# Kernel optimization log

Hardware: AMD Instinct MI355X
Metric: run time of the kernel (lower is better)

The kernel has to match this reference:

```python
import jax, jax.numpy as jnp
import numpy as np

B, S = 32, 256          # batch, sequence
D = 128                 # d_model
I = 256                 # mamba intermediate = 2*D
N = 16                  # ssm state size
R = 8                   # dt rank = ceil(D/16)
K = 4                   # conv kernel
L = 4                   # num mamba layers
Z = 128                 # vib z_dim
FUT = 20                # future steps


def setup_inputs() -> dict:
    key = jax.random.key(0)
    ks = iter(jax.random.split(key, 40))

    def nrm(shape, scale=0.02):
        return jax.random.normal(next(ks), shape, dtype=jnp.float32) * scale

    return {
        "x_cam": jax.random.normal(next(ks), (B, S, 8, 1024), dtype=jnp.float32),
        "x_ego": jax.random.normal(next(ks), (B, S, 64), dtype=jnp.float32),
        "vib_eps": jax.random.normal(next(ks), (B, Z), dtype=jnp.float32),
        "vis_w1": nrm((8 * 1024, 512)), "vis_b1": jnp.zeros((512,), jnp.float32),
        "vis_w2": nrm((512, D)), "vis_b2": jnp.zeros((D,), jnp.float32),
        "ego_w": nrm((64, D)), "ego_b": jnp.zeros((D,), jnp.float32),
        "fus_w": nrm((2 * D, D)), "fus_b": jnp.zeros((D,), jnp.float32),
        "norm_w": jnp.ones((L, D), jnp.float32),
        "in_proj_w": nrm((L, D, 2 * I)),
        "conv_w": nrm((L, I, K), 0.1), "conv_b": jnp.zeros((L, I), jnp.float32),
        "x_proj_w": nrm((L, I, R + 2 * N)),
        "dt_proj_w": nrm((L, R, I), 0.1), "dt_proj_b": jnp.full((L, I), -2.0, jnp.float32),
        "A_log": jnp.tile(jnp.log(jnp.arange(1, N + 1, dtype=jnp.float32))[None, None, :], (L, I, 1)),
        "D_par": jnp.ones((L, I), jnp.float32),
        "out_proj_w": nrm((L, I, D)),
        "normf_w": jnp.ones((D,), jnp.float32),
        "mu_w": nrm((D, Z)), "mu_b": jnp.zeros((Z,), jnp.float32),
        "lv_w": nrm((D, Z)), "lv_b": jnp.zeros((Z,), jnp.float32),
        "h1_w": nrm((Z, 256)), "h1_b": jnp.zeros((256,), jnp.float32),
        "h2_w": nrm((256, FUT * 2)), "h2_b": jnp.zeros((FUT * 2,), jnp.float32),
    }


def _rms(x, w, eps=1e-5):
    return x * jax.lax.rsqrt(jnp.mean(x * x, axis=-1, keepdims=True) + eps) * w


def _mixer(x, inw, cw, cb, xpw, dtw, dtb, alog, dpar, outw):
    # x: [B,S,D]
    Bb, Ss, _ = x.shape
    h, gate = jnp.split(x @ inw, 2, axis=-1)            # [B,S,I] each
    # depthwise causal conv (kernel K)
    hp = jnp.pad(h, ((0, 0), (K - 1, 0), (0, 0)))
    h = sum(hp[:, k:k + Ss, :] * cw[:, k] for k in range(K)) + cb
    h = jax.nn.silu(h)
    ssm = h @ xpw                                        # [B,S,R+2N]
    dt = jax.nn.softplus(ssm[..., :R] @ dtw + dtb)       # [B,S,I]
    Bm = ssm[..., R:R + N]                               # [B,S,N]
    Cm = ssm[..., R + N:]                                # [B,S,N]
    A = -jnp.exp(alog)                                   # [I,N]
    dA = jnp.exp(dt[..., None] * A)                      # [B,S,I,N]
    dBu = dt[..., None] * Bm[:, :, None, :] * h[..., None]  # [B,S,I,N]

    def step(carry, t):
        dA_t, dBu_t, C_t = t
        carry = carry * dA_t + dBu_t                     # [B,I,N]
        return carry, jnp.einsum('bin,bn->bi', carry, C_t)

    h0 = jnp.zeros((Bb, I, N), dtype=x.dtype)
    _, ys = jax.lax.scan(step, h0, (dA.swapaxes(0, 1), dBu.swapaxes(0, 1), Cm.swapaxes(0, 1)))
    y = ys.swapaxes(0, 1) + h * dpar                     # [B,S,I]
    y = y * jax.nn.silu(gate)
    return y @ outw                                      # [B,S,D]


def _mamba(x, norm_w, in_proj_w, conv_w, conv_b, x_proj_w, dt_proj_w, dt_proj_b, A_log, D_par, out_proj_w, normf_w):
    for l in range(L):
        x = x + _mixer(_rms(x, norm_w[l]), in_proj_w[l], conv_w[l], conv_b[l],
                       x_proj_w[l], dt_proj_w[l], dt_proj_b[l], A_log[l], D_par[l], out_proj_w[l])
    return _rms(x, normf_w)


def _forward(x_cam, x_ego, vib_eps, vis_w1, vis_b1, vis_w2, vis_b2, ego_w, ego_b, fus_w, fus_b,
             norm_w, in_proj_w, conv_w, conv_b, x_proj_w, dt_proj_w, dt_proj_b, A_log, D_par,
             out_proj_w, normf_w, mu_w, mu_b, lv_w, lv_b, h1_w, h1_b, h2_w, h2_b):
    Bb, Ss = x_cam.shape[:2]
    v = x_cam.reshape(Bb, Ss, -1)                                          # [B,S,8192]
    v = jax.nn.gelu(v @ vis_w1 + vis_b1, approximate=False) @ vis_w2 + vis_b2
    e = x_ego @ ego_w + ego_b
    fused = jax.nn.gelu(jnp.concatenate([v, e], axis=-1) @ fus_w + fus_b, approximate=False)
    h = _mamba(fused, norm_w, in_proj_w, conv_w, conv_b, x_proj_w,
               dt_proj_w, dt_proj_b, A_log, D_par, out_proj_w, normf_w)
    last = h[:, -1, :]                                                     # [B,D]
    mu = last @ mu_w + mu_b
    logvar = last @ lv_w + lv_b
    z = mu + vib_eps * jnp.exp(0.5 * logvar)
    kl = -0.5 * jnp.mean(1.0 + logvar - mu * mu - jnp.exp(logvar))
    out = jax.nn.relu(z @ h1_w + h1_b) @ h2_w + h2_b
    return out.reshape(Bb, FUT, 2), kl


def reference(x_cam, x_ego, vib_eps, vis_w1, vis_b1, vis_w2, vis_b2, ego_w, ego_b, fus_w, fus_b,
              norm_w, in_proj_w, conv_w, conv_b, x_proj_w, dt_proj_w, dt_proj_b, A_log, D_par,
              out_proj_w, normf_w, mu_w, mu_b, lv_w, lv_b, h1_w, h1_b, h2_w, h2_b):
    return _forward(x_cam, x_ego, vib_eps, vis_w1, vis_b1, vis_w2, vis_b2, ego_w, ego_b, fus_w, fus_b,
                    norm_w, in_proj_w, conv_w, conv_b, x_proj_w, dt_proj_w, dt_proj_b, A_log, D_par,
                    out_proj_w, normf_w, mu_w, mu_b, lv_w, lv_b, h1_w, h1_b, h2_w, h2_b)
```

## Files before the change

kernel.cpp:

```cpp
#include <hip/hip_runtime.h>
#include <hip/hip_bf16.h>
#include <math.h>

#define BQ 32
#define SQ 256
#define MTOK 8192
#define DD 128
#define II 256
#define NNs 16
#define RRs 8
#define KKs 4
#define LLs 4
#define ZZs 128
#define FUTs 20

typedef __attribute__((ext_vector_type(8))) short bf8v;
typedef __attribute__((ext_vector_type(4))) float f4v;

__device__ __forceinline__ float geluf(float x){ return 0.5f*x*(1.0f+erff(x*0.70710678118654752f)); }
__device__ __forceinline__ float siluf(float x){ return x/(1.0f+__expf(-x)); }
__device__ __forceinline__ float softplusf(float x){ return fmaxf(x,0.0f)+log1pf(__expf(-fabsf(x))); }
__device__ __forceinline__ unsigned short f2bf(float x){
    __hip_bfloat16 h = __float2bfloat16(x);
    return *reinterpret_cast<unsigned short*>(&h);
}

__device__ __forceinline__ void gload_lds16(const void* g, void* l){
    __builtin_amdgcn_global_load_lds(
        (const __attribute__((address_space(1))) void*)g,
        (__attribute__((address_space(3))) void*)l, 16, 0, 0);
}

#define PIPE_WAIT_BAR(N) do {                                   \
    __builtin_amdgcn_sched_barrier(0);                          \
    asm volatile("s_waitcnt vmcnt(" #N ")" ::: "memory");       \
    __builtin_amdgcn_s_barrier();                               \
    __builtin_amdgcn_sched_barrier(0);                          \
} while(0)

#define PIPE_END_BAR() do {                                     \
    __builtin_amdgcn_sched_barrier(0);                          \
    asm volatile("s_waitcnt lgkmcnt(0)" ::: "memory");          \
    __builtin_amdgcn_s_barrier();                               \
    __builtin_amdgcn_sched_barrier(0);                          \
} while(0)

template<int ACT,int ADD,int OUTBF>
__launch_bounds__(256,1)
__global__ void gemm_lds128_kernel(const unsigned short* __restrict__ A,
                                   const unsigned short* __restrict__ Bt,
                                   const float* __restrict__ bias,
                                   void* __restrict__ Cv,
                                   int M, int N, int Kd, int ldc)
{
    __shared__ __align__(16) unsigned short As[3][128*64];
    __shared__ __align__(16) unsigned short Bs[3][128*64];
    const int tid = threadIdx.x;
    const int w = tid >> 6, lane = tid & 63;
    const int ml = lane & 15, quad = lane >> 4;
    const int wm = w >> 1, wn = w & 1;
    const int rowBase = blockIdx.x * 128, colBase = blockIdx.y * 128;

    const int srow = w*8 + (lane>>3);
    const int scol = (((lane&7) ^ (lane>>3)))*8;

    f4v acc[4][4];
    #pragma unroll
    for (int i=0;i<4;i++)
      #pragma unroll
      for (int j=0;j<4;j++) acc[i][j] = (f4v){0.f,0.f,0.f,0.f};

    auto stage = [&](int buf, int kt){
        #pragma unroll
        for (int e=0;e<4;e++){
            const unsigned short* src = A + (size_t)(rowBase + srow + e*32)*Kd + kt + scol;
            gload_lds16(src, (unsigned short*)As[buf] + (w + e*4)*512);
        }
        #pragma unroll
        for (int e=0;e<4;e++){
            const unsigned short* src = Bt + (size_t)(colBase + srow + e*32)*Kd + kt + scol;
            gload_lds16(src, (unsigned short*)Bs[buf] + (w + e*4)*512);
        }
    };

    const int swz = (ml&7)*8;

    auto compute = [&](int buf){
        #pragma unroll
        for (int ks=0; ks<2; ks++){
            const int co = (ks*32 + quad*8) ^ swz;
            bf8v a[4], b[4];
            #pragma unroll
            for (int mf=0; mf<4; mf++)
                a[mf] = *reinterpret_cast<const bf8v*>(&As[buf][(wm*64 + mf*16 + ml)*64 + co]);
            #pragma unroll
            for (int nf=0; nf<4; nf++)
                b[nf] = *reinterpret_cast<const bf8v*>(&Bs[buf][(wn*64 + nf*16 + ml)*64 + co]);
            #pragma unroll
            for (int mf=0; mf<4; mf++)
                #pragma unroll
                for (int nf=0; nf<4; nf++)
                    acc[mf][nf] = __builtin_amdgcn_mfma_f32_16x16x32_bf16(a[mf], b[nf], acc[mf][nf], 0,0,0);
        }
    };

    const int nIter = Kd >> 6;
    stage(0, 0);
    stage(1, 64);

    int i = 0;
    for (; i + 2 < nIter; ++i){
        stage((i+2)%3, (i+2)<<6);
        PIPE_WAIT_BAR(16);
        compute(i%3);
        PIPE_END_BAR();
    }
    PIPE_WAIT_BAR(8);
    compute(i%3);
    PIPE_END_BAR();
    ++i;
    PIPE_WAIT_BAR(0);
    compute(i%3);

    #pragma unroll
    for (int mf=0; mf<4; mf++){
        #pragma unroll
        for (int nf=0; nf<4; nf++){
            int col = colBase + wn*64 + nf*16 + ml;
            float bb = bias ? bias[col] : 0.0f;
            #pragma unroll
            for (int r=0;r<4;r++){
                int row = rowBase + wm*64 + mf*16 + quad*4 + r;
                float v = acc[mf][nf][r] + bb;
                if (ACT==1) v = geluf(v);
                if constexpr (OUTBF==1){
                    ((unsigned short*)Cv)[(size_t)row*ldc + col] = f2bf(v);
                } else {
                    float* cp = (float*)Cv + (size_t)row*ldc + col;
                    if (ADD) v += *cp;
                    *cp = v;
                }
            }
        }
    }
}

template<int ACT,int ADD,int OUTBF>
__launch_bounds__(256,2)
__global__ void gemm_lds_kernel(const unsigned short* __restrict__ A,
                                const unsigned short* __restrict__ Bt,
                                const float* __restrict__ bias,
                                void* __restrict__ Cv,
                                int M, int N, int Kd, int ldc)
{
    __shared__ __align__(16) unsigned short As[3][128*64];
    __shared__ __align__(16) unsigned short Bs[3][64*64];
    const int tid = threadIdx.x;
    const int w = tid >> 6, lane = tid & 63;
    const int ml = lane & 15, quad = lane >> 4;
    const int rowBase = blockIdx.x * 128, colBase = blockIdx.y * 64;

    const int srow = w*8 + (lane>>3);
    const int scol = (((lane&7) ^ (lane>>3)))*8;

    f4v acc[2][4];
    #pragma unroll
    for (int i=0;i<2;i++)
      #pragma unroll
      for (int j=0;j<4;j++) acc[i][j] = (f4v){0.f,0.f,0.f,0.f};

    auto stage = [&](int buf, int kt){
        #pragma unroll
        for (int e=0;e<4;e++){
            const unsigned short* src = A + (size_t)(rowBase + srow + e*32)*Kd + kt + scol;
            gload_lds16(src, (unsigned short*)As[buf] + (w + e*4)*512);
        }
        #pragma unroll
        for (int e=0;e<2;e++){
            const unsigned short* src = Bt + (size_t)(colBase + srow + e*32)*Kd + kt + scol;
            gload_lds16(src, (unsigned short*)Bs[buf] + (w + e*4)*512);
        }
    };

    const int swz = (ml&7)*8;

    auto compute = [&](int buf){
        #pragma unroll
        for (int ks=0; ks<2; ks++){
            const int co = (ks*32 + quad*8) ^ swz;
            bf8v a0 = *reinterpret_cast<const bf8v*>(&As[buf][(w*32 +      ml)*64 + co]);
            bf8v a1 = *reinterpret_cast<const bf8v*>(&As[buf][(w*32 + 16 + ml)*64 + co]);
            #pragma unroll
            for (int nt=0; nt<4; nt++){
                bf8v b = *reinterpret_cast<const bf8v*>(&Bs[buf][(nt*16+ml)*64 + co]);
                acc[0][nt] = __builtin_amdgcn_mfma_f32_16x16x32_bf16(a0, b, acc[0][nt], 0,0,0);
                acc[1][nt] = __builtin_amdgcn_mfma_f32_16x16x32_bf16(a1, b, acc[1][nt], 0,0,0);
            }
        }
    };

    const int nIter = Kd >> 6;
    stage(0, 0);
    stage(1, 64);

    int i = 0;
    for (; i + 2 < nIter; ++i){
        stage((i+2)%3, (i+2)<<6);
        PIPE_WAIT_BAR(12);
        compute(i%3);
        PIPE_END_BAR();
    }
    PIPE_WAIT_BAR(6);
    compute(i%3);
    PIPE_END_BAR();
    ++i;
    PIPE_WAIT_BAR(0);
    compute(i%3);

    #pragma unroll
    for (int mt=0; mt<2; mt++){
        #pragma unroll
        for (int nt=0; nt<4; nt++){
            int col = colBase + nt*16 + ml;
            float bb = bias ? bias[col] : 0.0f;
            #pragma unroll
            for (int r=0;r<4;r++){
                int row = rowBase + w*32 + mt*16 + quad*4 + r;
                float v = acc[mt][nt][r] + bb;
                if (ACT==1) v = geluf(v);
                if constexpr (OUTBF==1){
                    ((unsigned short*)Cv)[(size_t)row*ldc + col] = f2bf(v);
                } else {
                    float* cp = (float*)Cv + (size_t)row*ldc + col;
                    if (ADD) v += *cp;
                    *cp = v;
                }
            }
        }
    }
}

template<int ACT,int ADD,int OUTBF,typename AT>
__launch_bounds__(256,2)
__global__ void gemm_bf16_kernel(const AT* __restrict__ A,
                                 const unsigned short* __restrict__ Bt,
                                 const float* __restrict__ bias,
                                 void* __restrict__ Cv,
                                 int M, int N, int Kd, int ldc)
{
    constexpr int LDK = 72;
    __shared__ unsigned short As[128*LDK];
    __shared__ unsigned short Bs[64*LDK];
    const int tid = threadIdx.x;
    const int w = tid >> 6, lane = tid & 63;
    const int ml = lane & 15, quad = lane >> 4;
    const int rowBase = blockIdx.x * 128, colBase = blockIdx.y * 64;

    f4v acc[2][4];
    #pragma unroll
    for (int i=0;i<2;i++)
      #pragma unroll
      for (int j=0;j<4;j++) acc[i][j] = (f4v){0.f,0.f,0.f,0.f};

    bf8v pa[4], pb[2];
    const int ar = tid >> 3, as8 = (tid & 7) * 8;

    auto loadTile = [&](int kt){
        #pragma unroll
        for (int e=0;e<4;e++){
            int r = ar + e*32;
            if constexpr (sizeof(AT)==2){
                pa[e] = *reinterpret_cast<const bf8v*>(
                    (const unsigned short*)A + (size_t)(rowBase+r)*Kd + kt + as8);
            } else {
                const float* ap = (const float*)A + (size_t)(rowBase+r)*Kd + kt + as8;
                float4 v0 = *reinterpret_cast<const float4*>(ap);
                float4 v1 = *reinterpret_cast<const float4*>(ap+4);
                union { unsigned short u[8]; bf8v v; } o;
                o.u[0]=f2bf(v0.x); o.u[1]=f2bf(v0.y); o.u[2]=f2bf(v0.z); o.u[3]=f2bf(v0.w);
                o.u[4]=f2bf(v1.x); o.u[5]=f2bf(v1.y); o.u[6]=f2bf(v1.z); o.u[7]=f2bf(v1.w);
                pa[e] = o.v;
            }
        }
        #pragma unroll
        for (int e=0;e<2;e++){
            int r = ar + e*32;
            pb[e] = *reinterpret_cast<const bf8v*>(
                Bt + (size_t)(colBase+r)*Kd + kt + as8);
        }
    };

    loadTile(0);

    for (int kt=0; kt<Kd; kt+=64){
        #pragma unroll
        for (int e=0;e<4;e++) *reinterpret_cast<bf8v*>(&As[(ar+e*32)*LDK + as8]) = pa[e];
        #pragma unroll
        for (int e=0;e<2;e++) *reinterpret_cast<bf8v*>(&Bs[(ar+e*32)*LDK + as8]) = pb[e];
        __syncthreads();
        if (kt + 64 < Kd) loadTile(kt + 64);
        #pragma unroll
        for (int ks=0; ks<2; ks++){
            bf8v a0 = *reinterpret_cast<bf8v*>(&As[(w*32 +      ml)*LDK + ks*32 + quad*8]);
            bf8v a1 = *reinterpret_cast<bf8v*>(&As[(w*32 + 16 + ml)*LDK + ks*32 + quad*8]);
            #pragma unroll
            for (int nt=0; nt<4; nt++){
                bf8v b = *reinterpret_cast<bf8v*>(&Bs[(nt*16+ml)*LDK + ks*32 + quad*8]);
                acc[0][nt] = __builtin_amdgcn_mfma_f32_16x16x32_bf16(a0, b, acc[0][nt], 0,0,0);
                acc[1][nt] = __builtin_amdgcn_mfma_f32_16x16x32_bf16(a1, b, acc[1][nt], 0,0,0);
            }
        }
        __syncthreads();
    }

    #pragma unroll
    for (int mt=0; mt<2; mt++){
        #pragma unroll
        for (int nt=0; nt<4; nt++){
            int col = colBase + nt*16 + ml;
            float bb = bias ? bias[col] : 0.0f;
            #pragma unroll
            for (int r=0;r<4;r++){
                int row = rowBase + w*32 + mt*16 + quad*4 + r;
                float v = acc[mt][nt][r] + bb;
                if (ACT==1) v = geluf(v);
                if constexpr (OUTBF==1){
                    ((unsigned short*)Cv)[(size_t)row*ldc + col] = f2bf(v);
                } else {
                    float* cp = (float*)Cv + (size_t)row*ldc + col;
                    if (ADD) v += *cp;
                    *cp = v;
                }
            }
        }
    }
}

__launch_bounds__(256)
__global__ void cast_bf16_kernel(const float* __restrict__ in, unsigned short* __restrict__ out)
{
    size_t i = (size_t)blockIdx.x*256 + threadIdx.x;
    const float4 v0 = reinterpret_cast<const float4*>(in)[i*2];
    const float4 v1 = reinterpret_cast<const float4*>(in)[i*2+1];
    union { unsigned short u[8]; bf8v v; } o;
    o.u[0]=f2bf(v0.x); o.u[1]=f2bf(v0.y); o.u[2]=f2bf(v0.z); o.u[3]=f2bf(v0.w);
    o.u[4]=f2bf(v1.x); o.u[5]=f2bf(v1.y); o.u[6]=f2bf(v1.z); o.u[7]=f2bf(v1.w);
    reinterpret_cast<bf8v*>(out)[i] = o.v;
}

__launch_bounds__(256)
__global__ void castT_kernel(const float* __restrict__ in, unsigned short* __restrict__ out,
                             int Kd, int N)
{
    __shared__ float t[64][65];
    int k0 = blockIdx.y*64, n0 = blockIdx.x*64;
    int c = threadIdx.x & 63, r4 = threadIdx.x >> 6;
    #pragma unroll
    for (int it=0; it<16; it++){
        int row = it*4 + r4;
        t[row][c] = in[(size_t)(k0+row)*N + n0 + c];
    }
    __syncthreads();
    #pragma unroll
    for (int it=0; it<16; it++){
        int row = it*4 + r4;
        out[(size_t)(n0+row)*Kd + k0 + c] = f2bf(t[c][row]);
    }
}

__launch_bounds__(256)
__global__ void rms_bf_kernel(const float* __restrict__ x, const float* __restrict__ w,
                              unsigned short* __restrict__ out)
{
    int tid = threadIdx.x;
    int lane = tid & 63, wv = tid >> 6;
    int token = blockIdx.x*4 + wv;
    const float* xr = x + (size_t)token*DD;
    float v0 = xr[lane], v1 = xr[lane+64];
    float ss = v0*v0 + v1*v1;
    #pragma unroll
    for (int off=32; off>0; off>>=1) ss += __shfl_xor(ss, off);
    float r = rsqrtf(ss*(1.0f/DD) + 1e-5f);
    unsigned short* o = out + (size_t)token*DD;
    o[lane]    = f2bf(v0*r*w[lane]);
    o[lane+64] = f2bf(v1*r*w[lane+64]);
}

__launch_bounds__(256)
__global__ void conv_kernel(const float* __restrict__ hg, const float* __restrict__ cw,
                            const float* __restrict__ cb, float* __restrict__ hc)
{
    int idx = blockIdx.x*256 + threadIdx.x;
    int i = idx & (II-1);
    int m = idx >> 8;
    int s = m & (SQ-1);
    const float* w = cw + i*KKs;
    float a = cb[i];
    #pragma unroll
    for (int k=0;k<KKs;k++){
        int ssrc = s + k - (KKs-1);
        if (ssrc >= 0) a += hg[(size_t)(m + k - (KKs-1))*(2*II) + i] * w[k];
    }
    hc[idx] = siluf(a);
}

#define XT 16
__launch_bounds__(256)
__global__ void xproj_fused_kernel(const float* __restrict__ hconv,
                                   const float* __restrict__ xpw,
                                   const float* __restrict__ dtw,
                                   const float* __restrict__ dtb,
                                   float* __restrict__ dt_out,
                                   float* __restrict__ bc)
{
    __shared__ float sh[XT][II+4];
    __shared__ float ssm_s[XT][40];
    const int tid = threadIdx.x;
    const int m0 = blockIdx.x * XT;

    {
        const float4* src = reinterpret_cast<const float4*>(hconv + (size_t)m0*II);
        #pragma unroll
        for (int e=0;e<4;e++){
            int idx = e*256 + tid;
            int t = idx >> 6, c = idx & 63;
            *reinterpret_cast<float4*>(&sh[t][c*4]) = src[idx];
        }
    }
    __syncthreads();

    for (int e = tid; e < XT*40; e += 256){
        int t = e / 40, o = e - t*40;
        float a0=0.f, a1=0.f, a2=0.f, a3=0.f;
        #pragma unroll 16
        for (int k=0;k<II;k+=4){
            float4 h4 = *reinterpret_cast<const float4*>(&sh[t][k]);
            a0 += h4.x*xpw[(k+0)*40+o];
            a1 += h4.y*xpw[(k+1)*40+o];
            a2 += h4.z*xpw[(k+2)*40+o];
            a3 += h4.w*xpw[(k+3)*40+o];
        }
        ssm_s[t][o] = (a0+a1)+(a2+a3);
    }
    __syncthreads();

    #pragma unroll
    for (int e = tid; e < XT*32; e += 256){
        int t = e >> 5, n = e & 31;
        bc[(size_t)(m0+t)*32 + n] = ssm_s[t][8+n];
    }

    {
        const int i = tid;
        float wr[RRs];
        #pragma unroll
        for (int r=0;r<RRs;r++) wr[r] = dtw[r*II + i];
        const float bb = dtb[i];
        #pragma unroll 4
        for (int t=0;t<XT;t++){
            float a = bb;
            #pragma unroll
            for (int r=0;r<RRs;r++) a += ssm_s[t][r]*wr[r];
            dt_out[(size_t)(m0+t)*II + i] = softplusf(a);
        }
    }
}

__launch_bounds__(256)
__global__ void scan_kernel(const float* __restrict__ dtp, const float* __restrict__ bc,
                            const float* __restrict__ hconv, const float* __restrict__ hg,
                            const float* __restrict__ A_log, const float* __restrict__ D_par,
                            unsigned short* __restrict__ ybf)
{
    __shared__ float sdt[16][17], shv[16][17], sgv[16][17], sbc[16][33];
    int b = blockIdx.x >> 4, chunk = blockIdx.x & 15;
    int tid = threadIdx.x;
    int n = tid & 15, il = tid >> 4;
    int i = chunk*16 + il;
    float A2 = -__expf(A_log[i*NNs + n]) * 1.44269504f;
    float carry = 0.0f;
    const float dpi = D_par[i];
    const int m0 = b*SQ;
    const int li = tid & 15, ls = tid >> 4;
    const int gi = chunk*16 + li;
    for (int cs=0; cs<16; cs++){
        __syncthreads();
        int mload = m0 + cs*16 + ls;
        sdt[ls][li] = dtp[(size_t)mload*II + gi];
        shv[ls][li] = hconv[(size_t)mload*II + gi];
        sgv[ls][li] = hg[(size_t)mload*(2*II) + II + gi];
        sbc[ls][li]      = bc[(size_t)mload*32 + li];
        sbc[ls][li + 16] = bc[(size_t)mload*32 + 16 + li];
        __syncthreads();
        #pragma unroll
        for (int s=0; s<16; s++){
            float dtv = sdt[s][il];
            float hv  = shv[s][il];
            float dA  = exp2f(dtv*A2);
            carry = carry*dA + dtv*hv*sbc[s][n];
            float acc = carry*sbc[s][16+n];
            acc += __shfl_xor(acc, 1);
            acc += __shfl_xor(acc, 2);
            acc += __shfl_xor(acc, 4);
            acc += __shfl_xor(acc, 8);
            if (n == 0){
                ybf[(size_t)(m0 + cs*16 + s)*II + i] =
                    f2bf((acc + hv*dpi) * siluf(sgv[s][il]));
            }
        }
    }
}

__launch_bounds__(128)
__global__ void head_kernel(const float* __restrict__ x, const float* __restrict__ normf,
                            const float* __restrict__ mu_w, const float* __restrict__ mu_b,
                            const float* __restrict__ lv_w, const float* __restrict__ lv_b,
                            const float* __restrict__ eps, const float* __restrict__ h1_w,
                            const float* __restrict__ h1_b, const float* __restrict__ h2_w,
                            const float* __restrict__ h2_b, float* __restrict__ out,
                            float* __restrict__ klacc)
{
    __shared__ float lasts[DD];
    __shared__ float zs[DD];
    __shared__ float hr[256];
    __shared__ float red[2];
    int b = blockIdx.x, d = threadIdx.x;
    int lane = d & 63, wv = d >> 6;
    float xv = x[((size_t)(b*SQ + SQ-1))*DD + d];
    float ss = xv*xv;
    #pragma unroll
    for (int off=32; off>0; off>>=1) ss += __shfl_xor(ss, off);
    if (lane==0) red[wv] = ss;
    __syncthreads();
    float tot = red[0] + red[1];
    float last = xv * rsqrtf(tot*(1.0f/DD) + 1e-5f) * normf[d];
    lasts[d] = last;
    __syncthreads();
    float mu = mu_b[d], lv = lv_b[d];
    for (int j=0;j<DD;j++){
        float lj = lasts[j];
        mu += lj*mu_w[j*DD + d];
        lv += lj*lv_w[j*DD + d];
    }
    float z = mu + eps[b*ZZs + d]*__expf(0.5f*lv);
    zs[d] = z;
    float klp = 1.0f + lv - mu*mu - __expf(lv);
    #pragma unroll
    for (int off=32; off>0; off>>=1) klp += __shfl_xor(klp, off);
    if (lane==0) red[wv] = klp;
    __syncthreads();
    if (d==0) atomicAdd(klacc, red[0]+red[1]);
    for (int o=d; o<256; o+=128){
        float a = h1_b[o];
        for (int j=0;j<DD;j++) a += zs[j]*h1_w[j*256 + o];
        hr[o] = fmaxf(a, 0.0f);
    }
    __syncthreads();
    if (d < 40){
        float a = h2_b[d];
        for (int k=0;k<256;k++) a += hr[k]*h2_w[k*40 + d];
        out[b*(FUTs*2) + d] = a;
    }
}

__global__ void kl_final_kernel(const float* __restrict__ klacc, float* __restrict__ out)
{
    out[0] = -0.5f * klacc[0] * (1.0f/(BQ*ZZs));
}

extern "C" void kernel_launch(void* const* d_in, const int* in_sizes, int n_in,
                              void* d_out, int out_size, void* d_ws, size_t ws_size,
                              hipStream_t stream)
{
    const float* x_cam     = (const float*)d_in[0];
    const float* x_ego     = (const float*)d_in[1];
    const float* vib_eps   = (const float*)d_in[2];
    const float* vis_w1    = (const float*)d_in[3];
    const float* vis_b1    = (const float*)d_in[4];
    const float* vis_w2    = (const float*)d_in[5];
    const float* vis_b2    = (const float*)d_in[6];
    const float* ego_w     = (const float*)d_in[7];
    const float* ego_b     = (const float*)d_in[8];
    const float* fus_w     = (const float*)d_in[9];
    const float* fus_b     = (const float*)d_in[10];
    const float* norm_w    = (const float*)d_in[11];
    const float* in_proj_w = (const float*)d_in[12];
    const float* conv_w    = (const float*)d_in[13];
    const float* conv_b    = (const float*)d_in[14];
    const float* x_proj_w  = (const float*)d_in[15];
    const float* dt_proj_w = (const float*)d_in[16];
    const float* dt_proj_b = (const float*)d_in[17];
    const float* A_log     = (const float*)d_in[18];
    const float* D_par     = (const float*)d_in[19];
    const float* out_proj_w= (const float*)d_in[20];
    const float* normf_w   = (const float*)d_in[21];
    const float* mu_w      = (const float*)d_in[22];
    const float* mu_b      = (const float*)d_in[23];
    const float* lv_w      = (const float*)d_in[24];
    const float* lv_b      = (const float*)d_in[25];
    const float* h1_w      = (const float*)d_in[26];
    const float* h1_b      = (const float*)d_in[27];
    const float* h2_w      = (const float*)d_in[28];
    const float* h2_b      = (const float*)d_in[29];

    float* ws = (float*)d_ws;
    float* hg    = ws;
    unsigned short* v1g  = (unsigned short*)hg;
    float* hconv = ws + 4194304;
    unsigned short* catbf = (unsigned short*)hconv;
    float* xbuf  = ws + 6291456;
    float* dtws  = ws + 7340032;
    float* bcws  = ws + 9437184;
    unsigned short* ybf  = (unsigned short*)(ws + 9699328);
    unsigned short* xnbf = (unsigned short*)(ws + 10747904);
    unsigned short* w1t  = (unsigned short*)(ws + 11272192);
    unsigned short* w2t  = (unsigned short*)(ws + 13369344);
    unsigned short* egot = (unsigned short*)(ws + 13402112);
    unsigned short* fust = (unsigned short*)(ws + 13406208);
    unsigned short* wipt = (unsigned short*)(ws + 13422592);
    unsigned short* wopt = (unsigned short*)(ws + 13553664);
    float* klacc = ws + 13619200;
    unsigned short* xcbf = (unsigned short*)(ws + 13619208);
    const size_t need_bytes = (size_t)(13619208 + 33554432) * 4;
    const bool big_ws = (ws_size >= need_bytes);

    hipMemsetAsync(klacc, 0, sizeof(float), stream);

    castT_kernel<<<dim3(8, 128), 256, 0, stream>>>(vis_w1, w1t, 8192, 512);
    castT_kernel<<<dim3(2, 8),   256, 0, stream>>>(vis_w2, w2t, 512, 128);
    castT_kernel<<<dim3(2, 1),   256, 0, stream>>>(ego_w,  egot, 64, 128);
    castT_kernel<<<dim3(2, 4),   256, 0, stream>>>(fus_w,  fust, 256, 128);
    for (int l=0; l<LLs; l++){
        castT_kernel<<<dim3(8, 2), 256, 0, stream>>>(
            in_proj_w + (size_t)l*DD*2*II, wipt + (size_t)l*2*II*DD, DD, 2*II);
        castT_kernel<<<dim3(2, 4), 256, 0, stream>>>(
            out_proj_w + (size_t)l*II*DD, wopt + (size_t)l*DD*II, II, DD);
    }

    if (big_ws){
        cast_bf16_kernel<<<32768, 256, 0, stream>>>(x_cam, xcbf);
        gemm_lds128_kernel<1,0,1><<<dim3(64, 4), 256, 0, stream>>>(
            xcbf, w1t, vis_b1, v1g, MTOK, 512, 8192, 512);
    } else {
        gemm_bf16_kernel<1,0,1,float><<<dim3(64, 8), 256, 0, stream>>>(
            x_cam, w1t, vis_b1, v1g, MTOK, 512, 8192, 512);
    }
    gemm_lds_kernel<0,0,1><<<dim3(64, 2), 256, 0, stream>>>(
        v1g, w2t, vis_b2, catbf, MTOK, 128, 512, 256);
    gemm_bf16_kernel<0,0,1,float><<<dim3(64, 2), 256, 0, stream>>>(
        x_ego, egot, ego_b, catbf + 128, MTOK, 128, 64, 256);
    gemm_lds_kernel<1,0,0><<<dim3(64, 2), 256, 0, stream>>>(
        catbf, fust, fus_b, xbuf, MTOK, 128, 256, 128);

    for (int l=0; l<LLs; l++){
        rms_bf_kernel<<<MTOK/4, 256, 0, stream>>>(xbuf, norm_w + l*DD, xnbf);
        gemm_lds128_kernel<0,0,0><<<dim3(64, 4), 256, 0, stream>>>(
            xnbf, wipt + (size_t)l*2*II*DD, nullptr, hg, MTOK, 2*II, DD, 2*II);
        conv_kernel<<<MTOK*II/256, 256, 0, stream>>>(
            hg, conv_w + (size_t)l*II*KKs, conv_b + (size_t)l*II, hconv);
        xproj_fused_kernel<<<MTOK/XT, 256, 0, stream>>>(
            hconv, x_proj_w + (size_t)l*II*40, dt_proj_w + (size_t)l*RRs*II,
            dt_proj_b + (size_t)l*II, dtws, bcws);
        scan_kernel<<<BQ*16, 256, 0, stream>>>(
            dtws, bcws, hconv, hg, A_log + (size_t)l*II*NNs, D_par + (size_t)l*II, ybf);
        gemm_lds_kernel<0,1,0><<<dim3(64, 2), 256, 0, stream>>>(
            ybf, wopt + (size_t)l*DD*II, nullptr, xbuf, MTOK, DD, II, DD);
    }

    head_kernel<<<BQ, 128, 0, stream>>>(
        xbuf, normf_w, mu_w, mu_b, lv_w, lv_b, vib_eps,
        h1_w, h1_b, h2_w, h2_b, (float*)d_out, klacc);
    kl_final_kernel<<<1, 1, 0, stream>>>(klacc, (float*)d_out + 1280);
}
```

Baseline: 1.250 ms.

## Use 512-thread 128x128 GEMM and 64x64-tile GEMM for narrow projections

The 128x128-tile GEMM now runs with 512 threads (8 waves, each computing a 64x32 sub-tile), so more waves per CU can hide latency while the LDS tiling stays the same. The narrow-N GEMMs switch from 128x64 to 64x64 tiles, doubling the grid to 256 blocks so the CUs are better filled. Wait counts are adjusted to match the new number of loads per stage. Smaller tiles lower data reuse per block and add more redundant B-tile loads.

```diff
diff --git a/kernel.cpp b/kernel.cpp
--- a/kernel.cpp
+++ b/kernel.cpp
@@ -46,40 +46,38 @@
 } while(0)
 
 template<int ACT,int ADD,int OUTBF>
-__launch_bounds__(256,1)
-__global__ void gemm_lds128_kernel(const unsigned short* __restrict__ A,
-                                   const unsigned short* __restrict__ Bt,
-                                   const float* __restrict__ bias,
-                                   void* __restrict__ Cv,
-                                   int M, int N, int Kd, int ldc)
+__launch_bounds__(512,1)
+__global__ void gemm_w512_kernel(const unsigned short* __restrict__ A,
+                                 const unsigned short* __restrict__ Bt,
+                                 const float* __restrict__ bias,
+                                 void* __restrict__ Cv,
+                                 int M, int N, int Kd, int ldc)
 {
     __shared__ __align__(16) unsigned short As[3][128*64];
     __shared__ __align__(16) unsigned short Bs[3][128*64];
     const int tid = threadIdx.x;
     const int w = tid >> 6, lane = tid & 63;
     const int ml = lane & 15, quad = lane >> 4;
-    const int wm = w >> 1, wn = w & 1;
+    const int wm = w >> 2, wn = w & 3;
     const int rowBase = blockIdx.x * 128, colBase = blockIdx.y * 128;
 
-    const int srow = w*8 + (lane>>3);
+    const int srow = lane >> 3;
     const int scol = (((lane&7) ^ (lane>>3)))*8;
 
-    f4v acc[4][4];
+    f4v acc[4][2];
     #pragma unroll
     for (int i=0;i<4;i++)
       #pragma unroll
-      for (int j=0;j<4;j++) acc[i][j] = (f4v){0.f,0.f,0.f,0.f};
+      for (int j=0;j<2;j++) acc[i][j] = (f4v){0.f,0.f,0.f,0.f};
 
     auto stage = [&](int buf, int kt){
         #pragma unroll
-        for (int e=0;e<4;e++){
-            const unsigned short* src = A + (size_t)(rowBase + srow + e*32)*Kd + kt + scol;
-            gload_lds16(src, (unsigned short*)As[buf] + (w + e*4)*512);
-        }
-        #pragma unroll
-        for (int e=0;e<4;e++){
-            const unsigned short* src = Bt + (size_t)(colBase + srow + e*32)*Kd + kt + scol;
-            gload_lds16(src, (unsigned short*)Bs[buf] + (w + e*4)*512);
+        for (int e=0;e<2;e++){
+            const int c = w*2 + e;
+            const unsigned short* srcA = A + (size_t)(rowBase + c*8 + srow)*Kd + kt + scol;
+            gload_lds16(srcA, (unsigned short*)As[buf] + c*512);
+            const unsigned short* srcB = Bt + (size_t)(colBase + c*8 + srow)*Kd + kt + scol;
+            gload_lds16(srcB, (unsigned short*)Bs[buf] + c*512);
         }
     };
 
@@ -89,17 +87,17 @@
         #pragma unroll
         for (int ks=0; ks<2; ks++){
             const int co = (ks*32 + quad*8) ^ swz;
-            bf8v a[4], b[4];
+            bf8v a[4], b[2];
             #pragma unroll
             for (int mf=0; mf<4; mf++)
                 a[mf] = *reinterpret_cast<const bf8v*>(&As[buf][(wm*64 + mf*16 + ml)*64 + co]);
             #pragma unroll
-            for (int nf=0; nf<4; nf++)
-                b[nf] = *reinterpret_cast<const bf8v*>(&Bs[buf][(wn*64 + nf*16 + ml)*64 + co]);
+            for (int nf=0; nf<2; nf++)
+                b[nf] = *reinterpret_cast<const bf8v*>(&Bs[buf][(wn*32 + nf*16 + ml)*64 + co]);
             #pragma unroll
             for (int mf=0; mf<4; mf++)
                 #pragma unroll
-                for (int nf=0; nf<4; nf++)
+                for (int nf=0; nf<2; nf++)
                     acc[mf][nf] = __builtin_amdgcn_mfma_f32_16x16x32_bf16(a[mf], b[nf], acc[mf][nf], 0,0,0);
         }
     };
@@ -111,11 +109,11 @@
     int i = 0;
     for (; i + 2 < nIter; ++i){
         stage((i+2)%3, (i+2)<<6);
-        PIPE_WAIT_BAR(16);
+        PIPE_WAIT_BAR(8);
         compute(i%3);
         PIPE_END_BAR();
     }
-    PIPE_WAIT_BAR(8);
+    PIPE_WAIT_BAR(4);
     compute(i%3);
     PIPE_END_BAR();
     ++i;
@@ -125,8 +123,8 @@
     #pragma unroll
     for (int mf=0; mf<4; mf++){
         #pragma unroll
-        for (int nf=0; nf<4; nf++){
-            int col = colBase + wn*64 + nf*16 + ml;
+        for (int nf=0; nf<2; nf++){
+            int col = colBase + wn*32 + nf*16 + ml;
             float bb = bias ? bias[col] : 0.0f;
             #pragma unroll
             for (int r=0;r<4;r++){
@@ -147,38 +145,34 @@
 
 template<int ACT,int ADD,int OUTBF>
 __launch_bounds__(256,2)
-__global__ void gemm_lds_kernel(const unsigned short* __restrict__ A,
-                                const unsigned short* __restrict__ Bt,
-                                const float* __restrict__ bias,
-                                void* __restrict__ Cv,
-                                int M, int N, int Kd, int ldc)
-{
-    __shared__ __align__(16) unsigned short As[3][128*64];
+__global__ void gemm_lds64_kernel(const unsigned short* __restrict__ A,
+                                  const unsigned short* __restrict__ Bt,
+                                  const float* __restrict__ bias,
+                                  void* __restrict__ Cv,
+                                  int M, int N, int Kd, int ldc)
+{
+    __shared__ __align__(16) unsigned short As[3][64*64];
     __shared__ __align__(16) unsigned short Bs[3][64*64];
     const int tid = threadIdx.x;
     const int w = tid >> 6, lane = tid & 63;
     const int ml = lane & 15, quad = lane >> 4;
-    const int rowBase = blockIdx.x * 128, colBase = blockIdx.y * 64;
-
-    const int srow = w*8 + (lane>>3);
+    const int rowBase = blockIdx.x * 64, colBase = blockIdx.y * 64;
+
+    const int srow = lane >> 3;
     const int scol = (((lane&7) ^ (lane>>3)))*8;
 
-    f4v acc[2][4];
-    #pragma unroll
-    for (int i=0;i<2;i++)
-      #pragma unroll
-      for (int j=0;j<4;j++) acc[i][j] = (f4v){0.f,0.f,0.f,0.f};
+    f4v acc[4];
+    #pragma unroll
+    for (int j=0;j<4;j++) acc[j] = (f4v){0.f,0.f,0.f,0.f};
 
     auto stage = [&](int buf, int kt){
         #pragma unroll
-        for (int e=0;e<4;e++){
-            const unsigned short* src = A + (size_t)(rowBase + srow + e*32)*Kd + kt + scol;
-            gload_lds16(src, (unsigned short*)As[buf] + (w + e*4)*512);
-        }
-        #pragma unroll
         for (int e=0;e<2;e++){
-            const unsigned short* src = Bt + (size_t)(colBase + srow + e*32)*Kd + kt + scol;
-            gload_lds16(src, (unsigned short*)Bs[buf] + (w + e*4)*512);
+            const int c = w*2 + e;
+            const unsigned short* srcA = A + (size_t)(rowBase + c*8 + srow)*Kd + kt + scol;
+            gload_lds16(srcA, (unsigned short*)As[buf] + c*512);
+            const unsigned short* srcB = Bt + (size_t)(colBase + c*8 + srow)*Kd + kt + scol;
+            gload_lds16(srcB, (unsigned short*)Bs[buf] + c*512);
         }
     };
 
@@ -188,13 +182,11 @@
         #pragma unroll
         for (int ks=0; ks<2; ks++){
             const int co = (ks*32 + quad*8) ^ swz;
-            bf8v a0 = *reinterpret_cast<const bf8v*>(&As[buf][(w*32 +      ml)*64 + co]);
-            bf8v a1 = *reinterpret_cast<const bf8v*>(&As[buf][(w*32 + 16 + ml)*64 + co]);
+            bf8v a0 = *reinterpret_cast<const bf8v*>(&As[buf][(w*16 + ml)*64 + co]);
             #pragma unroll
             for (int nt=0; nt<4; nt++){
                 bf8v b = *reinterpret_cast<const bf8v*>(&Bs[buf][(nt*16+ml)*64 + co]);
-                acc[0][nt] = __builtin_amdgcn_mfma_f32_16x16x32_bf16(a0, b, acc[0][nt], 0,0,0);
-                acc[1][nt] = __builtin_amdgcn_mfma_f32_16x16x32_bf16(a1, b, acc[1][nt], 0,0,0);
+                acc[nt] = __builtin_amdgcn_mfma_f32_16x16x32_bf16(a0, b, acc[nt], 0,0,0);
             }
         }
     };
@@ -206,11 +198,11 @@
     int i = 0;
     for (; i + 2 < nIter; ++i){
         stage((i+2)%3, (i+2)<<6);
-        PIPE_WAIT_BAR(12);
+        PIPE_WAIT_BAR(8);
         compute(i%3);
         PIPE_END_BAR();
     }
-    PIPE_WAIT_BAR(6);
+    PIPE_WAIT_BAR(4);
     compute(i%3);
     PIPE_END_BAR();
     ++i;
@@ -218,23 +210,20 @@
     compute(i%3);
 
     #pragma unroll
-    for (int mt=0; mt<2; mt++){
-        #pragma unroll
-        for (int nt=0; nt<4; nt++){
-            int col = colBase + nt*16 + ml;
-            float bb = bias ? bias[col] : 0.0f;
-            #pragma unroll
-            for (int r=0;r<4;r++){
-                int row = rowBase + w*32 + mt*16 + quad*4 + r;
-                float v = acc[mt][nt][r] + bb;
-                if (ACT==1) v = geluf(v);
-                if constexpr (OUTBF==1){
-                    ((unsigned short*)Cv)[(size_t)row*ldc + col] = f2bf(v);
-                } else {
-                    float* cp = (float*)Cv + (size_t)row*ldc + col;
-                    if (ADD) v += *cp;
-                    *cp = v;
-                }
+    for (int nt=0; nt<4; nt++){
+        int col = colBase + nt*16 + ml;
+        float bb = bias ? bias[col] : 0.0f;
+        #pragma unroll
+        for (int r=0;r<4;r++){
+            int row = rowBase + w*16 + quad*4 + r;
+            float v = acc[nt][r] + bb;
+            if (ACT==1) v = geluf(v);
+            if constexpr (OUTBF==1){
+                ((unsigned short*)Cv)[(size_t)row*ldc + col] = f2bf(v);
+            } else {
+                float* cp = (float*)Cv + (size_t)row*ldc + col;
+                if (ADD) v += *cp;
+                *cp = v;
             }
         }
     }
@@ -639,22 +628,22 @@
 
     if (big_ws){
         cast_bf16_kernel<<<32768, 256, 0, stream>>>(x_cam, xcbf);
-        gemm_lds128_kernel<1,0,1><<<dim3(64, 4), 256, 0, stream>>>(
+        gemm_w512_kernel<1,0,1><<<dim3(64, 4), 512, 0, stream>>>(
             xcbf, w1t, vis_b1, v1g, MTOK, 512, 8192, 512);
     } else {
         gemm_bf16_kernel<1,0,1,float><<<dim3(64, 8), 256, 0, stream>>>(
             x_cam, w1t, vis_b1, v1g, MTOK, 512, 8192, 512);
     }
-    gemm_lds_kernel<0,0,1><<<dim3(64, 2), 256, 0, stream>>>(
+    gemm_lds64_kernel<0,0,1><<<dim3(128, 2), 256, 0, stream>>>(
         v1g, w2t, vis_b2, catbf, MTOK, 128, 512, 256);
     gemm_bf16_kernel<0,0,1,float><<<dim3(64, 2), 256, 0, stream>>>(
         x_ego, egot, ego_b, catbf + 128, MTOK, 128, 64, 256);
-    gemm_lds_kernel<1,0,0><<<dim3(64, 2), 256, 0, stream>>>(
+    gemm_lds64_kernel<1,0,0><<<dim3(128, 2), 256, 0, stream>>>(
         catbf, fust, fus_b, xbuf, MTOK, 128, 256, 128);
 
     for (int l=0; l<LLs; l++){
         rms_bf_kernel<<<MTOK/4, 256, 0, stream>>>(xbuf, norm_w + l*DD, xnbf);
-        gemm_lds128_kernel<0,0,0><<<dim3(64, 4), 256, 0, stream>>>(
+        gemm_w512_kernel<0,0,0><<<dim3(64, 4), 512, 0, stream>>>(
             xnbf, wipt + (size_t)l*2*II*DD, nullptr, hg, MTOK, 2*II, DD, 2*II);
         conv_kernel<<<MTOK*II/256, 256, 0, stream>>>(
             hg, conv_w + (size_t)l*II*KKs, conv_b + (size_t)l*II, hconv);
@@ -663,7 +652,7 @@
             dt_proj_b + (size_t)l*II, dtws, bcws);
         scan_kernel<<<BQ*16, 256, 0, stream>>>(
             dtws, bcws, hconv, hg, A_log + (size_t)l*II*NNs, D_par + (size_t)l*II, ybf);
-        gemm_lds_kernel<0,1,0><<<dim3(64, 2), 256, 0, stream>>>(
+        gemm_lds64_kernel<0,1,0><<<dim3(128, 2), 256, 0, stream>>>(
             ybf, wopt + (size_t)l*DD*II, nullptr, xbuf, MTOK, DD, II, DD);
     }
 
```

Measured after the change: 1.228 ms. No clear change (-1.8%).
